# Optimization experiments

Measured on AMD Instinct MI355X. Metric: run time of the kernel, lower is better.

The kernel has to match this reference:

```python
import jax, jax.numpy as jnp
import numpy as np

HEADS = 4
DIM_HEAD = 32


def setup_inputs() -> dict:
    key = jax.random.key(0)
    k1, k2, k3 = jax.random.split(key, 3)
    dim = 128
    hidden = HEADS * DIM_HEAD  # 128
    x = jax.random.normal(k1, (2, dim, 16, 16, 16), dtype=jnp.float32)
    # 1x1x1 Conv3d weights are pointwise linear maps: store as [out, in]
    w_qkv = jax.random.normal(k2, (hidden * 3, dim), dtype=jnp.float32) * (1.0 / np.sqrt(dim))
    w_out = jax.random.normal(k3, (dim, hidden), dtype=jnp.float32) * (1.0 / np.sqrt(hidden))
    b_out = jnp.zeros((dim,), dtype=jnp.float32)
    return {"x": x, "w_qkv": w_qkv, "w_out": w_out, "b_out": b_out}


def reference(x, w_qkv, w_out, b_out):
    b, c, D, H, W = x.shape
    N = D * H * W
    scale = DIM_HEAD ** -0.5
    # to_qkv: 1x1x1 conv == pointwise channel matmul
    qkv = jnp.einsum('oc,bcdhw->bodhw', w_qkv, x)  # [b, 3*heads*dim_head, D, H, W]
    q, k, v = jnp.split(qkv, 3, axis=1)
    # 'b (h c) d x y -> b h c (d x y)'
    q = q.reshape(b, HEADS, DIM_HEAD, N) * scale
    k = k.reshape(b, HEADS, DIM_HEAD, N)
    v = v.reshape(b, HEADS, DIM_HEAD, N)
    sim = jnp.einsum('bhdi,bhdj->bhij', q, k)      # [b, h, N, N]
    attn = jax.nn.softmax(sim, axis=-1)             # max-subtraction folded in
    out = jnp.einsum('bhij,bhdj->bhid', attn, v)    # [b, h, N, dim_head]
    # 'b h (d x y) d1 -> b (h d1) d x y'
    out = out.reshape(b, HEADS, D, H, W, DIM_HEAD)
    out = out.transpose(0, 1, 5, 2, 3, 4).reshape(b, HEADS * DIM_HEAD, D, H, W)
    # to_out: 1x1x1 conv with bias
    y = jnp.einsum('oc,bcdhw->bodhw', w_out, out) + b_out[None, :, None, None, None]
    return y
```

## Files before the change

kernel.cpp:

```cpp
#include <hip/hip_runtime.h>
#include <hip/hip_bf16.h>
#include <math.h>

typedef __attribute__((ext_vector_type(8))) __bf16 bf16x8;
typedef __attribute__((ext_vector_type(4))) __bf16 bf16x4;
typedef __attribute__((ext_vector_type(4))) float f32x4;

#define NTOK 4096
#define DHEAD 32
#define MBIAS 12.0f
#define QSCALE 0.2550316626f

static __device__ __forceinline__ float fexp2(float x) {
    return __builtin_amdgcn_exp2f(x);
}

__global__ __launch_bounds__(256, 4) void qkv_mfma_kernel(const float* __restrict__ x,
                                                          const float* __restrict__ w,
                                                          __bf16* __restrict__ Qo,
                                                          __bf16* __restrict__ Ko,
                                                          __bf16* __restrict__ Vo)
{
    const int bid   = blockIdx.x;
    const int ot    = bid % 6;
    const int ntile = bid / 6;
    const int tid   = threadIdx.x;
    const int wv    = tid >> 6, lane = tid & 63;
    const int g = lane >> 4, ql = lane & 15;
    const int o0 = ot * 64 + wv * 16;
    const int n0 = ntile * 32;

    f32x4 acc[2] = {{0.f,0.f,0.f,0.f},{0.f,0.f,0.f,0.f}};

    #pragma unroll
    for (int kc = 0; kc < 4; ++kc) {
        const float* wp = w + (size_t)(o0 + ql) * 128 + kc * 32 + g * 8;
        f32x4 w0 = *(const f32x4*)wp;
        f32x4 w1 = *(const f32x4*)(wp + 4);
        bf16x8 wh, wl;
        #pragma unroll
        for (int i = 0; i < 4; ++i) {
            float v0 = w0[i], v1 = w1[i];
            __bf16 h0 = (__bf16)v0, h1 = (__bf16)v1;
            wh[i] = h0; wh[4 + i] = h1;
            wl[i] = (__bf16)(v0 - (float)h0);
            wl[4 + i] = (__bf16)(v1 - (float)h1);
        }
        #pragma unroll
        for (int nt = 0; nt < 2; ++nt) {
            const int ng = n0 + nt * 16 + ql;
            const int b = ng >> 12, nn = ng & (NTOK - 1);
            const float* xp = x + ((size_t)b * 128 + kc * 32 + g * 8) * NTOK + nn;
            bf16x8 bh, bl;
            #pragma unroll
            for (int i = 0; i < 8; ++i) {
                float v = xp[(size_t)i * NTOK];
                __bf16 h = (__bf16)v;
                bh[i] = h;
                bl[i] = (__bf16)(v - (float)h);
            }
            acc[nt] = __builtin_amdgcn_mfma_f32_16x16x32_bf16(wh, bh, acc[nt], 0, 0, 0);
            acc[nt] = __builtin_amdgcn_mfma_f32_16x16x32_bf16(wl, bh, acc[nt], 0, 0, 0);
            acc[nt] = __builtin_amdgcn_mfma_f32_16x16x32_bf16(wh, bl, acc[nt], 0, 0, 0);
        }
    }

    const int orow = o0 + 4 * g;
    #pragma unroll
    for (int nt = 0; nt < 2; ++nt) {
        const int ng = n0 + nt * 16 + ql;
        const int b = ng >> 12, nn = ng & (NTOK - 1);
        if (orow < 128) {
            const int h = orow >> 5, d0 = orow & 31;
            bf16x4 q4;
            #pragma unroll
            for (int r = 0; r < 4; ++r) q4[r] = (__bf16)(acc[nt][r] * QSCALE);
            *(bf16x4*)(Qo + ((size_t)(b * 4 + h) * NTOK + nn) * DHEAD + d0) = q4;
        } else if (orow < 256) {
            const int oo = orow - 128, h = oo >> 5, d0 = oo & 31;
            bf16x4 k4;
            #pragma unroll
            for (int r = 0; r < 4; ++r) k4[r] = (__bf16)acc[nt][r];
            *(bf16x4*)(Ko + ((size_t)(b * 4 + h) * NTOK + nn) * DHEAD + d0) = k4;
        } else {
            const int oo = orow - 256, h = oo >> 5, d0 = oo & 31;
            #pragma unroll
            for (int r = 0; r < 4; ++r)
                Vo[((size_t)(b * 4 + h) * DHEAD + d0 + r) * NTOK + nn] = (__bf16)acc[nt][r];
        }
    }
}

__global__ __launch_bounds__(512, 4) void attn_kernel(const __bf16* __restrict__ Q,
                                                      const __bf16* __restrict__ K,
                                                      const __bf16* __restrict__ VT,
                                                      float* __restrict__ ot)
{
    __shared__ float red[8][2048];
    __shared__ float redl[8][64];
    const int bid = blockIdx.x;
    const int bh  = bid & 7;
    const int qg  = bid >> 3;
    const int tid = threadIdx.x;
    const int wv  = tid >> 6;
    const int lane = tid & 63;
    const int g = lane >> 4, ql = lane & 15;
    const __bf16* Qb = Q  + (size_t)bh * NTOK * DHEAD;
    const __bf16* Kb = K  + (size_t)bh * NTOK * DHEAD;
    const __bf16* Vb = VT + (size_t)bh * DHEAD * NTOK;
    const int q0 = qg * 64;

    bf16x8 qf[4];
    #pragma unroll
    for (int qt = 0; qt < 4; ++qt)
        qf[qt] = *(const bf16x8*)(Qb + (size_t)(q0 + qt * 16 + ql) * DHEAD + 8 * g);

    f32x4 acc[4][2] = {};
    float lsum[4] = {0.f, 0.f, 0.f, 0.f};
    const f32x4 mneg = {-MBIAS, -MBIAS, -MBIAS, -MBIAS};

    const __bf16* krow  = Kb + (size_t)ql * DHEAD + 8 * g;
    const __bf16* vrow0 = Vb + (size_t)ql * NTOK;
    const __bf16* vrow1 = Vb + (size_t)(16 + ql) * NTOK;

    const int base = wv * 512;
    for (int kv0 = base; kv0 < base + 512; kv0 += 32) {
        bf16x8 kf0 = *(const bf16x8*)(krow + (size_t)kv0 * DHEAD);
        bf16x8 kf1 = *(const bf16x8*)(krow + (size_t)(kv0 + 16) * DHEAD);
        bf16x4 va00 = *(const bf16x4*)(vrow0 + kv0 + 4 * g);
        bf16x4 va01 = *(const bf16x4*)(vrow0 + kv0 + 16 + 4 * g);
        bf16x4 va10 = *(const bf16x4*)(vrow1 + kv0 + 4 * g);
        bf16x4 va11 = *(const bf16x4*)(vrow1 + kv0 + 16 + 4 * g);
        bf16x8 vf0 = __builtin_shufflevector(va00, va01, 0,1,2,3,4,5,6,7);
        bf16x8 vf1 = __builtin_shufflevector(va10, va11, 0,1,2,3,4,5,6,7);

        #pragma unroll
        for (int qt = 0; qt < 4; ++qt) {
            f32x4 s0 = __builtin_amdgcn_mfma_f32_16x16x32_bf16(kf0, qf[qt], mneg, 0, 0, 0);
            f32x4 s1 = __builtin_amdgcn_mfma_f32_16x16x32_bf16(kf1, qf[qt], mneg, 0, 0, 0);
            bf16x8 pf;
            float ps = 0.f;
            #pragma unroll
            for (int r = 0; r < 4; ++r) {
                float e0 = fexp2(s0[r]);
                float e1 = fexp2(s1[r]);
                ps += e0 + e1;
                pf[r]     = (__bf16)e0;
                pf[4 + r] = (__bf16)e1;
            }
            lsum[qt] += ps;
            acc[qt][0] = __builtin_amdgcn_mfma_f32_16x16x32_bf16(vf0, pf, acc[qt][0], 0, 0, 0);
            acc[qt][1] = __builtin_amdgcn_mfma_f32_16x16x32_bf16(vf1, pf, acc[qt][1], 0, 0, 0);
        }
    }

    #pragma unroll
    for (int qt = 0; qt < 4; ++qt) {
        lsum[qt] += __shfl_xor(lsum[qt], 16);
        lsum[qt] += __shfl_xor(lsum[qt], 32);
    }

    #pragma unroll
    for (int qt = 0; qt < 4; ++qt)
        #pragma unroll
        for (int dt = 0; dt < 2; ++dt)
            #pragma unroll
            for (int r = 0; r < 4; ++r)
                red[wv][(qt * 8 + dt * 4 + r) * 64 + lane] = acc[qt][dt][r];
    if (lane < 16) {
        #pragma unroll
        for (int qt = 0; qt < 4; ++qt) redl[wv][qt * 16 + ql] = lsum[qt];
    }
    __syncthreads();

    {
        const int e0 = tid * 4;
        float s0 = 0.f, s1 = 0.f, s2 = 0.f, s3 = 0.f;
        #pragma unroll
        for (int w = 0; w < 8; ++w) {
            s0 += red[w][e0];     s1 += red[w][e0 + 1];
            s2 += red[w][e0 + 2]; s3 += red[w][e0 + 3];
        }
        red[0][e0] = s0; red[0][e0 + 1] = s1; red[0][e0 + 2] = s2; red[0][e0 + 3] = s3;
        if (tid < 64) {
            float s = 0.f;
            #pragma unroll
            for (int w = 0; w < 8; ++w) s += redl[w][tid];
            redl[0][tid] = s;
        }
    }
    __syncthreads();

    if (wv < 4) {
        const int qt = wv;
        float* otb = ot + (size_t)bh * 32 * NTOK + q0;
        const float inv = 1.0f / redl[0][qt * 16 + ql];
        #pragma unroll
        for (int dt = 0; dt < 2; ++dt)
            #pragma unroll
            for (int r = 0; r < 4; ++r)
                otb[(size_t)(dt * 16 + 4 * g + r) * NTOK + qt * 16 + ql] =
                    red[0][(qt * 8 + dt * 4 + r) * 64 + lane] * inv;
    }
}

__global__ __launch_bounds__(256, 4) void out_mfma_kernel(const float* __restrict__ ot,
                                                          const float* __restrict__ w,
                                                          const float* __restrict__ bias,
                                                          float* __restrict__ y)
{
    const int bid   = blockIdx.x;
    const int otile = bid & 1;
    const int ntile = bid >> 1;
    const int tid   = threadIdx.x;
    const int wv    = tid >> 6, lane = tid & 63;
    const int g = lane >> 4, ql = lane & 15;
    const int o0 = otile * 64 + wv * 16;
    const int n0 = ntile * 16;

    f32x4 acc = {0.f,0.f,0.f,0.f};
    const int ng = n0 + ql;
    const int b = ng >> 12, nn = ng & (NTOK - 1);

    #pragma unroll
    for (int kc = 0; kc < 4; ++kc) {
        const float* wp = w + (size_t)(o0 + ql) * 128 + kc * 32 + g * 8;
        f32x4 w0 = *(const f32x4*)wp;
        f32x4 w1 = *(const f32x4*)(wp + 4);
        bf16x8 wh, wl;
        #pragma unroll
        for (int i = 0; i < 4; ++i) {
            float v0 = w0[i], v1 = w1[i];
            __bf16 h0 = (__bf16)v0, h1 = (__bf16)v1;
            wh[i] = h0; wh[4 + i] = h1;
            wl[i] = (__bf16)(v0 - (float)h0);
            wl[4 + i] = (__bf16)(v1 - (float)h1);
        }
        const float* op = ot + (((size_t)(b * 4 + kc)) * 32 + g * 8) * NTOK + nn;
        bf16x8 bh, bl;
        #pragma unroll
        for (int i = 0; i < 8; ++i) {
            float v = op[(size_t)i * NTOK];
            __bf16 h = (__bf16)v;
            bh[i] = h;
            bl[i] = (__bf16)(v - (float)h);
        }
        acc = __builtin_amdgcn_mfma_f32_16x16x32_bf16(wh, bh, acc, 0, 0, 0);
        acc = __builtin_amdgcn_mfma_f32_16x16x32_bf16(wl, bh, acc, 0, 0, 0);
        acc = __builtin_amdgcn_mfma_f32_16x16x32_bf16(wh, bl, acc, 0, 0, 0);
    }

    const int orow = o0 + 4 * g;
    #pragma unroll
    for (int r = 0; r < 4; ++r)
        y[((size_t)b * 128 + orow + r) * NTOK + nn] = acc[r] + bias[orow + r];
}

extern "C" void kernel_launch(void* const* d_in, const int* in_sizes, int n_in,
                              void* d_out, int out_size, void* d_ws, size_t ws_size,
                              hipStream_t stream) {
    const float* x     = (const float*)d_in[0];
    const float* w_qkv = (const float*)d_in[1];
    const float* w_out = (const float*)d_in[2];
    const float* b_out = (const float*)d_in[3];
    float* y = (float*)d_out;

    char* ws = (char*)d_ws;
    __bf16* Qb = (__bf16*)(ws);
    __bf16* Kb = (__bf16*)(ws + (size_t)2 * 1024 * 1024);
    __bf16* Vb = (__bf16*)(ws + (size_t)4 * 1024 * 1024);
    float*  ob = (float*)(ws + (size_t)6 * 1024 * 1024);

    hipLaunchKernelGGL(qkv_mfma_kernel, dim3(1536), dim3(256), 0, stream, x, w_qkv, Qb, Kb, Vb);
    hipLaunchKernelGGL(attn_kernel, dim3(512), dim3(512), 0, stream, Qb, Kb, Vb, ob);
    hipLaunchKernelGGL(out_mfma_kernel, dim3(1024), dim3(256), 0, stream, ob, w_out, b_out, y);
}
```

Baseline: 120.0 us.

## Pre-split inputs into token-major bf16 hi/lo buffers and prefetch K/V in attention

Adds a split kernel that converts x into token-major bf16 hi/lo arrays, so the QKV projection loads contiguous bf16x8 vectors instead of doing strided fp32 gathers and per-element splitting. The attention kernel now writes its output directly as token-major bf16 hi/lo pairs, so the output projection also reads contiguous vectors. The attention loop is software-pipelined to load the next K/V tile while computing the current one. The cost is an extra kernel launch, more workspace, and higher register pressure in the attention loop.

New measurement: 136.7 us. +13.9%, slower.

```diff
diff --git a/kernel.cpp b/kernel.cpp
--- a/kernel.cpp
+++ b/kernel.cpp
@@ -15,7 +15,35 @@
     return __builtin_amdgcn_exp2f(x);
 }
 
-__global__ __launch_bounds__(256, 4) void qkv_mfma_kernel(const float* __restrict__ x,
+__global__ __launch_bounds__(256) void split_x_kernel(const float* __restrict__ x,
+                                                      __bf16* __restrict__ xh,
+                                                      __bf16* __restrict__ xl)
+{
+    const int tid  = threadIdx.x;
+    const int w    = tid >> 6, lane = tid & 63;
+    const int n    = blockIdx.x * 128 + (w >> 1) * 64 + lane;
+    const int c0   = (w & 1) * 64;
+    const int b    = n >> 12;
+    const int nn   = n & (NTOK - 1);
+    const float* xp = x + ((size_t)b * 128 + c0) * NTOK + nn;
+    __bf16* hp = xh + (size_t)n * 128 + c0;
+    __bf16* lp = xl + (size_t)n * 128 + c0;
+    for (int i0 = 0; i0 < 64; i0 += 8) {
+        bf16x8 h8, l8;
+        #pragma unroll
+        for (int i = 0; i < 8; ++i) {
+            float v = xp[(size_t)(i0 + i) * NTOK];
+            __bf16 h = (__bf16)v;
+            h8[i] = h;
+            l8[i] = (__bf16)(v - (float)h);
+        }
+        *(bf16x8*)(hp + i0) = h8;
+        *(bf16x8*)(lp + i0) = l8;
+    }
+}
+
+__global__ __launch_bounds__(256, 4) void qkv_mfma_kernel(const __bf16* __restrict__ xh,
+                                                          const __bf16* __restrict__ xl,
                                                           const float* __restrict__ w,
                                                           __bf16* __restrict__ Qo,
                                                           __bf16* __restrict__ Ko,
@@ -48,17 +76,9 @@
         }
         #pragma unroll
         for (int nt = 0; nt < 2; ++nt) {
-            const int ng = n0 + nt * 16 + ql;
-            const int b = ng >> 12, nn = ng & (NTOK - 1);
-            const float* xp = x + ((size_t)b * 128 + kc * 32 + g * 8) * NTOK + nn;
-            bf16x8 bh, bl;
-            #pragma unroll
-            for (int i = 0; i < 8; ++i) {
-                float v = xp[(size_t)i * NTOK];
-                __bf16 h = (__bf16)v;
-                bh[i] = h;
-                bl[i] = (__bf16)(v - (float)h);
-            }
+            const size_t bofs = (size_t)(n0 + nt * 16 + ql) * 128 + kc * 32 + g * 8;
+            bf16x8 bh = *(const bf16x8*)(xh + bofs);
+            bf16x8 bl = *(const bf16x8*)(xl + bofs);
             acc[nt] = __builtin_amdgcn_mfma_f32_16x16x32_bf16(wh, bh, acc[nt], 0, 0, 0);
             acc[nt] = __builtin_amdgcn_mfma_f32_16x16x32_bf16(wl, bh, acc[nt], 0, 0, 0);
             acc[nt] = __builtin_amdgcn_mfma_f32_16x16x32_bf16(wh, bl, acc[nt], 0, 0, 0);
@@ -94,7 +114,8 @@
 __global__ __launch_bounds__(512, 4) void attn_kernel(const __bf16* __restrict__ Q,
                                                       const __bf16* __restrict__ K,
                                                       const __bf16* __restrict__ VT,
-                                                      float* __restrict__ ot)
+                                                      __bf16* __restrict__ oth,
+                                                      __bf16* __restrict__ otl)
 {
     __shared__ float red[8][2048];
     __shared__ float redl[8][64];
@@ -124,13 +145,22 @@
     const __bf16* vrow1 = Vb + (size_t)(16 + ql) * NTOK;
 
     const int base = wv * 512;
+    bf16x8 kf0 = *(const bf16x8*)(krow + (size_t)base * DHEAD);
+    bf16x8 kf1 = *(const bf16x8*)(krow + (size_t)(base + 16) * DHEAD);
+    bf16x4 va00 = *(const bf16x4*)(vrow0 + base + 4 * g);
+    bf16x4 va01 = *(const bf16x4*)(vrow0 + base + 16 + 4 * g);
+    bf16x4 va10 = *(const bf16x4*)(vrow1 + base + 4 * g);
+    bf16x4 va11 = *(const bf16x4*)(vrow1 + base + 16 + 4 * g);
+
     for (int kv0 = base; kv0 < base + 512; kv0 += 32) {
-        bf16x8 kf0 = *(const bf16x8*)(krow + (size_t)kv0 * DHEAD);
-        bf16x8 kf1 = *(const bf16x8*)(krow + (size_t)(kv0 + 16) * DHEAD);
-        bf16x4 va00 = *(const bf16x4*)(vrow0 + kv0 + 4 * g);
-        bf16x4 va01 = *(const bf16x4*)(vrow0 + kv0 + 16 + 4 * g);
-        bf16x4 va10 = *(const bf16x4*)(vrow1 + kv0 + 4 * g);
-        bf16x4 va11 = *(const bf16x4*)(vrow1 + kv0 + 16 + 4 * g);
+        const int kvn = base + ((kv0 + 32 - base) & 511);
+        bf16x8 nkf0 = *(const bf16x8*)(krow + (size_t)kvn * DHEAD);
+        bf16x8 nkf1 = *(const bf16x8*)(krow + (size_t)(kvn + 16) * DHEAD);
+        bf16x4 nva00 = *(const bf16x4*)(vrow0 + kvn + 4 * g);
+        bf16x4 nva01 = *(const bf16x4*)(vrow0 + kvn + 16 + 4 * g);
+        bf16x4 nva10 = *(const bf16x4*)(vrow1 + kvn + 4 * g);
+        bf16x4 nva11 = *(const bf16x4*)(vrow1 + kvn + 16 + 4 * g);
+
         bf16x8 vf0 = __builtin_shufflevector(va00, va01, 0,1,2,3,4,5,6,7);
         bf16x8 vf1 = __builtin_shufflevector(va10, va11, 0,1,2,3,4,5,6,7);
 
@@ -152,6 +182,9 @@
             acc[qt][0] = __builtin_amdgcn_mfma_f32_16x16x32_bf16(vf0, pf, acc[qt][0], 0, 0, 0);
             acc[qt][1] = __builtin_amdgcn_mfma_f32_16x16x32_bf16(vf1, pf, acc[qt][1], 0, 0, 0);
         }
+
+        kf0 = nkf0; kf1 = nkf1;
+        va00 = nva00; va01 = nva01; va10 = nva10; va11 = nva11;
     }
 
     #pragma unroll
@@ -193,18 +226,29 @@
 
     if (wv < 4) {
         const int qt = wv;
-        float* otb = ot + (size_t)bh * 32 * NTOK + q0;
+        const int b = bh >> 2, h = bh & 3;
+        const int n = q0 + qt * 16 + ql;
         const float inv = 1.0f / redl[0][qt * 16 + ql];
-        #pragma unroll
-        for (int dt = 0; dt < 2; ++dt)
-            #pragma unroll
-            for (int r = 0; r < 4; ++r)
-                otb[(size_t)(dt * 16 + 4 * g + r) * NTOK + qt * 16 + ql] =
-                    red[0][(qt * 8 + dt * 4 + r) * 64 + lane] * inv;
-    }
-}
-
-__global__ __launch_bounds__(256, 4) void out_mfma_kernel(const float* __restrict__ ot,
+        __bf16* hp = oth + ((size_t)b * NTOK + n) * 128 + h * 32;
+        __bf16* lp = otl + ((size_t)b * NTOK + n) * 128 + h * 32;
+        #pragma unroll
+        for (int dt = 0; dt < 2; ++dt) {
+            bf16x4 h4, l4;
+            #pragma unroll
+            for (int r = 0; r < 4; ++r) {
+                float v = red[0][(qt * 8 + dt * 4 + r) * 64 + lane] * inv;
+                __bf16 hh = (__bf16)v;
+                h4[r] = hh;
+                l4[r] = (__bf16)(v - (float)hh);
+            }
+            *(bf16x4*)(hp + dt * 16 + 4 * g) = h4;
+            *(bf16x4*)(lp + dt * 16 + 4 * g) = l4;
+        }
+    }
+}
+
+__global__ __launch_bounds__(256, 4) void out_mfma_kernel(const __bf16* __restrict__ oh,
+                                                          const __bf16* __restrict__ ol,
                                                           const float* __restrict__ w,
                                                           const float* __restrict__ bias,
                                                           float* __restrict__ y)
@@ -219,8 +263,6 @@
     const int n0 = ntile * 16;
 
     f32x4 acc = {0.f,0.f,0.f,0.f};
-    const int ng = n0 + ql;
-    const int b = ng >> 12, nn = ng & (NTOK - 1);
 
     #pragma unroll
     for (int kc = 0; kc < 4; ++kc) {
@@ -236,21 +278,17 @@
             wl[i] = (__bf16)(v0 - (float)h0);
             wl[4 + i] = (__bf16)(v1 - (float)h1);
         }
-        const float* op = ot + (((size_t)(b * 4 + kc)) * 32 + g * 8) * NTOK + nn;
-        bf16x8 bh, bl;
-        #pragma unroll
-        for (int i = 0; i < 8; ++i) {
-            float v = op[(size_t)i * NTOK];
-            __bf16 h = (__bf16)v;
-            bh[i] = h;
-            bl[i] = (__bf16)(v - (float)h);
-        }
+        const size_t bofs = (size_t)(n0 + ql) * 128 + kc * 32 + g * 8;
+        bf16x8 bh = *(const bf16x8*)(oh + bofs);
+        bf16x8 bl = *(const bf16x8*)(ol + bofs);
         acc = __builtin_amdgcn_mfma_f32_16x16x32_bf16(wh, bh, acc, 0, 0, 0);
         acc = __builtin_amdgcn_mfma_f32_16x16x32_bf16(wl, bh, acc, 0, 0, 0);
         acc = __builtin_amdgcn_mfma_f32_16x16x32_bf16(wh, bl, acc, 0, 0, 0);
     }
 
     const int orow = o0 + 4 * g;
+    const int ng = n0 + ql;
+    const int b = ng >> 12, nn = ng & (NTOK - 1);
     #pragma unroll
     for (int r = 0; r < 4; ++r)
         y[((size_t)b * 128 + orow + r) * NTOK + nn] = acc[r] + bias[orow + r];
@@ -266,12 +304,16 @@
     float* y = (float*)d_out;
 
     char* ws = (char*)d_ws;
-    __bf16* Qb = (__bf16*)(ws);
-    __bf16* Kb = (__bf16*)(ws + (size_t)2 * 1024 * 1024);
-    __bf16* Vb = (__bf16*)(ws + (size_t)4 * 1024 * 1024);
-    float*  ob = (float*)(ws + (size_t)6 * 1024 * 1024);
-
-    hipLaunchKernelGGL(qkv_mfma_kernel, dim3(1536), dim3(256), 0, stream, x, w_qkv, Qb, Kb, Vb);
-    hipLaunchKernelGGL(attn_kernel, dim3(512), dim3(512), 0, stream, Qb, Kb, Vb, ob);
-    hipLaunchKernelGGL(out_mfma_kernel, dim3(1024), dim3(256), 0, stream, ob, w_out, b_out, y);
-}
+    __bf16* xh  = (__bf16*)(ws);
+    __bf16* xl  = (__bf16*)(ws + (size_t)2 * 1024 * 1024);
+    __bf16* Qb  = (__bf16*)(ws + (size_t)4 * 1024 * 1024);
+    __bf16* Kb  = (__bf16*)(ws + (size_t)6 * 1024 * 1024);
+    __bf16* Vb  = (__bf16*)(ws + (size_t)8 * 1024 * 1024);
+    __bf16* oth = (__bf16*)(ws + (size_t)10 * 1024 * 1024);
+    __bf16* otl = (__bf16*)(ws + (size_t)12 * 1024 * 1024);
+
+    hipLaunchKernelGGL(split_x_kernel, dim3(64), dim3(256), 0, stream, x, xh, xl);
+    hipLaunchKernelGGL(qkv_mfma_kernel, dim3(1536), dim3(256), 0, stream, xh, xl, w_qkv, Qb, Kb, Vb);
+    hipLaunchKernelGGL(attn_kernel, dim3(512), dim3(512), 0, stream, Qb, Kb, Vb, oth, otl);
+    hipLaunchKernelGGL(out_mfma_kernel, dim3(1024), dim3(256), 0, stream, oth, otl, w_out, b_out, y);
+}
```

## Split KV across blocks with LDS-staged K/V tiles and separate combine kernel

Applied to the files above, without the earlier changes.

The attention kernel changes from each block handling 64 queries with 8 waves splitting the KV range to each block handling 512 queries (64 per wave) over one 512-token KV split. K and V tiles are staged cooperatively into swizzled, double-buffered LDS, so all waves share them instead of each wave reading them from global memory. Partial outputs and row sums go to workspace and a new combine kernel sums the splits and normalizes. This removes the in-block LDS reduction and the redundant K/V global loads, at the cost of an extra launch and extra global traffic for the partials (8x32x4096 floats per head).

Measured after the change: 155.5 us. 29.5% more time.

```diff
diff --git a/kernel.cpp b/kernel.cpp
--- a/kernel.cpp
+++ b/kernel.cpp
@@ -10,10 +10,13 @@
 #define DHEAD 32
 #define MBIAS 12.0f
 #define QSCALE 0.2550316626f
+#define NSP 8
 
 static __device__ __forceinline__ float fexp2(float x) {
     return __builtin_amdgcn_exp2f(x);
 }
+
+#define SWZ(byte, row) ((byte) ^ (((row) & 7) << 4))
 
 __global__ __launch_bounds__(256, 4) void qkv_mfma_kernel(const float* __restrict__ x,
                                                           const float* __restrict__ w,
@@ -94,13 +97,14 @@
 __global__ __launch_bounds__(512, 4) void attn_kernel(const __bf16* __restrict__ Q,
                                                       const __bf16* __restrict__ K,
                                                       const __bf16* __restrict__ VT,
-                                                      float* __restrict__ ot)
+                                                      float* __restrict__ opart,
+                                                      float* __restrict__ lpart)
 {
-    __shared__ float red[8][2048];
-    __shared__ float redl[8][64];
+    __shared__ __align__(16) char smem[2][8192];
     const int bid = blockIdx.x;
-    const int bh  = bid & 7;
-    const int qg  = bid >> 3;
+    const int sp  = bid & 7;
+    const int qb  = (bid >> 3) & 7;
+    const int bh  = bid >> 6;
     const int tid = threadIdx.x;
     const int wv  = tid >> 6;
     const int lane = tid & 63;
@@ -108,7 +112,22 @@
     const __bf16* Qb = Q  + (size_t)bh * NTOK * DHEAD;
     const __bf16* Kb = K  + (size_t)bh * NTOK * DHEAD;
     const __bf16* Vb = VT + (size_t)bh * DHEAD * NTOK;
-    const int q0 = qg * 64;
+    const int q0  = qb * 512 + wv * 64;
+    const int kv0 = sp * 512;
+
+    const __bf16* sSrc;
+    int sDst, sAdv;
+    if (tid < 256) {
+        const int row = tid >> 2, col = tid & 3;
+        sSrc = Kb + (size_t)(kv0 + row) * DHEAD + col * 8;
+        sDst = SWZ(row * 64 + col * 16, row);
+        sAdv = 64 * DHEAD;
+    } else {
+        const int t2 = tid - 256, row = t2 >> 3, col = t2 & 7;
+        sSrc = Vb + (size_t)row * NTOK + kv0 + col * 8;
+        sDst = 4096 + SWZ(row * 128 + col * 16, row);
+        sAdv = 64;
+    }
 
     bf16x8 qf[4];
     #pragma unroll
@@ -119,39 +138,51 @@
     float lsum[4] = {0.f, 0.f, 0.f, 0.f};
     const f32x4 mneg = {-MBIAS, -MBIAS, -MBIAS, -MBIAS};
 
-    const __bf16* krow  = Kb + (size_t)ql * DHEAD + 8 * g;
-    const __bf16* vrow0 = Vb + (size_t)ql * NTOK;
-    const __bf16* vrow1 = Vb + (size_t)(16 + ql) * NTOK;
-
-    const int base = wv * 512;
-    for (int kv0 = base; kv0 < base + 512; kv0 += 32) {
-        bf16x8 kf0 = *(const bf16x8*)(krow + (size_t)kv0 * DHEAD);
-        bf16x8 kf1 = *(const bf16x8*)(krow + (size_t)(kv0 + 16) * DHEAD);
-        bf16x4 va00 = *(const bf16x4*)(vrow0 + kv0 + 4 * g);
-        bf16x4 va01 = *(const bf16x4*)(vrow0 + kv0 + 16 + 4 * g);
-        bf16x4 va10 = *(const bf16x4*)(vrow1 + kv0 + 4 * g);
-        bf16x4 va11 = *(const bf16x4*)(vrow1 + kv0 + 16 + 4 * g);
-        bf16x8 vf0 = __builtin_shufflevector(va00, va01, 0,1,2,3,4,5,6,7);
-        bf16x8 vf1 = __builtin_shufflevector(va10, va11, 0,1,2,3,4,5,6,7);
-
-        #pragma unroll
-        for (int qt = 0; qt < 4; ++qt) {
-            f32x4 s0 = __builtin_amdgcn_mfma_f32_16x16x32_bf16(kf0, qf[qt], mneg, 0, 0, 0);
-            f32x4 s1 = __builtin_amdgcn_mfma_f32_16x16x32_bf16(kf1, qf[qt], mneg, 0, 0, 0);
-            bf16x8 pf;
-            float ps = 0.f;
-            #pragma unroll
-            for (int r = 0; r < 4; ++r) {
-                float e0 = fexp2(s0[r]);
-                float e1 = fexp2(s1[r]);
-                ps += e0 + e1;
-                pf[r]     = (__bf16)e0;
-                pf[4 + r] = (__bf16)e1;
+    bf16x8 sreg = *(const bf16x8*)sSrc;
+    *(bf16x8*)(smem[0] + sDst) = sreg;
+    __syncthreads();
+
+    for (int t = 0; t < 8; ++t) {
+        const int cur = t & 1;
+        if (t < 7) sreg = *(const bf16x8*)(sSrc + (size_t)(t + 1) * sAdv);
+        const char* kb  = smem[cur];
+        const char* vbp = smem[cur] + 4096;
+
+        #pragma unroll
+        for (int s = 0; s < 2; ++s) {
+            const int r0 = s * 32 + ql, r1 = s * 32 + 16 + ql;
+            bf16x8 kf0 = *(const bf16x8*)(kb + SWZ(r0 * 64 + g * 16, r0));
+            bf16x8 kf1 = *(const bf16x8*)(kb + SWZ(r1 * 64 + g * 16, r1));
+            const int voff = s * 64 + g * 8;
+            bf16x4 va00 = *(const bf16x4*)(vbp + SWZ(ql * 128 + voff, ql));
+            bf16x4 va01 = *(const bf16x4*)(vbp + SWZ(ql * 128 + voff + 32, ql));
+            bf16x4 va10 = *(const bf16x4*)(vbp + SWZ((16 + ql) * 128 + voff, 16 + ql));
+            bf16x4 va11 = *(const bf16x4*)(vbp + SWZ((16 + ql) * 128 + voff + 32, 16 + ql));
+            bf16x8 vf0 = __builtin_shufflevector(va00, va01, 0,1,2,3,4,5,6,7);
+            bf16x8 vf1 = __builtin_shufflevector(va10, va11, 0,1,2,3,4,5,6,7);
+
+            #pragma unroll
+            for (int qt = 0; qt < 4; ++qt) {
+                f32x4 s0 = __builtin_amdgcn_mfma_f32_16x16x32_bf16(kf0, qf[qt], mneg, 0, 0, 0);
+                f32x4 s1 = __builtin_amdgcn_mfma_f32_16x16x32_bf16(kf1, qf[qt], mneg, 0, 0, 0);
+                bf16x8 pf;
+                float ps = 0.f;
+                #pragma unroll
+                for (int r = 0; r < 4; ++r) {
+                    float e0 = fexp2(s0[r]);
+                    float e1 = fexp2(s1[r]);
+                    ps += e0 + e1;
+                    pf[r]     = (__bf16)e0;
+                    pf[4 + r] = (__bf16)e1;
+                }
+                lsum[qt] += ps;
+                acc[qt][0] = __builtin_amdgcn_mfma_f32_16x16x32_bf16(vf0, pf, acc[qt][0], 0, 0, 0);
+                acc[qt][1] = __builtin_amdgcn_mfma_f32_16x16x32_bf16(vf1, pf, acc[qt][1], 0, 0, 0);
             }
-            lsum[qt] += ps;
-            acc[qt][0] = __builtin_amdgcn_mfma_f32_16x16x32_bf16(vf0, pf, acc[qt][0], 0, 0, 0);
-            acc[qt][1] = __builtin_amdgcn_mfma_f32_16x16x32_bf16(vf1, pf, acc[qt][1], 0, 0, 0);
-        }
+        }
+
+        if (t < 7) *(bf16x8*)(smem[cur ^ 1] + sDst) = sreg;
+        __syncthreads();
     }
 
     #pragma unroll
@@ -160,48 +191,38 @@
         lsum[qt] += __shfl_xor(lsum[qt], 32);
     }
 
-    #pragma unroll
-    for (int qt = 0; qt < 4; ++qt)
+    float* ob = opart + (size_t)(sp * 8 + bh) * 32 * NTOK;
+    float* lp = lpart + (size_t)(sp * 8 + bh) * NTOK;
+    #pragma unroll
+    for (int qt = 0; qt < 4; ++qt) {
+        const int q = q0 + qt * 16 + ql;
         #pragma unroll
         for (int dt = 0; dt < 2; ++dt)
             #pragma unroll
             for (int r = 0; r < 4; ++r)
-                red[wv][(qt * 8 + dt * 4 + r) * 64 + lane] = acc[qt][dt][r];
-    if (lane < 16) {
-        #pragma unroll
-        for (int qt = 0; qt < 4; ++qt) redl[wv][qt * 16 + ql] = lsum[qt];
-    }
-    __syncthreads();
-
-    {
-        const int e0 = tid * 4;
-        float s0 = 0.f, s1 = 0.f, s2 = 0.f, s3 = 0.f;
-        #pragma unroll
-        for (int w = 0; w < 8; ++w) {
-            s0 += red[w][e0];     s1 += red[w][e0 + 1];
-            s2 += red[w][e0 + 2]; s3 += red[w][e0 + 3];
-        }
-        red[0][e0] = s0; red[0][e0 + 1] = s1; red[0][e0 + 2] = s2; red[0][e0 + 3] = s3;
-        if (tid < 64) {
-            float s = 0.f;
-            #pragma unroll
-            for (int w = 0; w < 8; ++w) s += redl[w][tid];
-            redl[0][tid] = s;
-        }
-    }
-    __syncthreads();
-
-    if (wv < 4) {
-        const int qt = wv;
-        float* otb = ot + (size_t)bh * 32 * NTOK + q0;
-        const float inv = 1.0f / redl[0][qt * 16 + ql];
-        #pragma unroll
-        for (int dt = 0; dt < 2; ++dt)
-            #pragma unroll
-            for (int r = 0; r < 4; ++r)
-                otb[(size_t)(dt * 16 + 4 * g + r) * NTOK + qt * 16 + ql] =
-                    red[0][(qt * 8 + dt * 4 + r) * 64 + lane] * inv;
-    }
+                ob[(size_t)(dt * 16 + 4 * g + r) * NTOK + q] = acc[qt][dt][r];
+        if (g == 0) lp[q] = lsum[qt];
+    }
+}
+
+__global__ __launch_bounds__(256) void combine_kernel(const float* __restrict__ opart,
+                                                      const float* __restrict__ lpart,
+                                                      float* __restrict__ ot)
+{
+    const int gid = blockIdx.x * 256 + threadIdx.x;
+    const int q   = (gid * 4) & (NTOK - 1);
+    const int row = gid >> 10;
+    const int bh  = row >> 5;
+    f32x4 l4 = {0.f,0.f,0.f,0.f}, o4 = {0.f,0.f,0.f,0.f};
+    #pragma unroll
+    for (int sp = 0; sp < NSP; ++sp) {
+        l4 += *(const f32x4*)(lpart + (size_t)(sp * 8 + bh) * NTOK + q);
+        o4 += *(const f32x4*)(opart + ((size_t)sp * 256 + row) * NTOK + q);
+    }
+    f32x4 r;
+    #pragma unroll
+    for (int i = 0; i < 4; ++i) r[i] = o4[i] / l4[i];
+    *(f32x4*)(ot + (size_t)row * NTOK + q) = r;
 }
 
 __global__ __launch_bounds__(256, 4) void out_mfma_kernel(const float* __restrict__ ot,
@@ -266,12 +287,15 @@
     float* y = (float*)d_out;
 
     char* ws = (char*)d_ws;
-    __bf16* Qb = (__bf16*)(ws);
-    __bf16* Kb = (__bf16*)(ws + (size_t)2 * 1024 * 1024);
-    __bf16* Vb = (__bf16*)(ws + (size_t)4 * 1024 * 1024);
-    float*  ob = (float*)(ws + (size_t)6 * 1024 * 1024);
+    __bf16* Qb    = (__bf16*)(ws);
+    __bf16* Kb    = (__bf16*)(ws + (size_t)2  * 1024 * 1024);
+    __bf16* Vb    = (__bf16*)(ws + (size_t)4  * 1024 * 1024);
+    float*  ob    = (float*) (ws + (size_t)6  * 1024 * 1024);
+    float*  lpart = (float*) (ws + (size_t)10 * 1024 * 1024);
+    float*  opart = (float*) (ws + (size_t)11 * 1024 * 1024);
 
     hipLaunchKernelGGL(qkv_mfma_kernel, dim3(1536), dim3(256), 0, stream, x, w_qkv, Qb, Kb, Vb);
-    hipLaunchKernelGGL(attn_kernel, dim3(512), dim3(512), 0, stream, Qb, Kb, Vb, ob);
+    hipLaunchKernelGGL(attn_kernel, dim3(512), dim3(512), 0, stream, Qb, Kb, Vb, opart, lpart);
+    hipLaunchKernelGGL(combine_kernel, dim3(1024), dim3(256), 0, stream, opart, lpart, ob);
     hipLaunchKernelGGL(out_mfma_kernel, dim3(1024), dim3(256), 0, stream, ob, w_out, b_out, y);
 }
```
